# Optimization experiments

Hardware: AMD Instinct MI355X
Metric: run time of the kernel (lower is better)

## Reference

```python
import jax, jax.numpy as jnp
import numpy as np

RATE = 0.5
POLICY = 3
FREQ_MASK = 15
TIME_MASK = 35


def setup_inputs() -> dict:
    key = jax.random.key(0)
    x = jax.random.normal(key, (64, 1, 4000, 128), dtype=jnp.float32)
    return {"x": x}


def _band_mask(key_apply, key_start, b, policy, length, width, rate):
    """Keep-mask [b, length]: True where NOT covered by any random band.

    Matches torch: apply if rand<rate; start = int(rand*(length-width)).
    """
    apply = jax.random.uniform(key_apply, (b, policy)) < rate            # [b,p]
    start = jnp.floor(jax.random.uniform(key_start, (b, policy))
                      * (length - width)).astype(jnp.int32)              # [b,p]
    pos = jnp.arange(length, dtype=jnp.int32)                            # [length]
    hit = (apply[:, :, None]
           & (pos[None, None, :] >= start[:, :, None])
           & (pos[None, None, :] < (start + width)[:, :, None]))        # [b,p,length]
    return ~jnp.any(hit, axis=1)                                         # [b,length]


def reference(x):
    b, c, t, f = x.shape
    kt_a, kt_s, kf_a, kf_s = jax.random.split(jax.random.key(1), 4)
    keep_t = _band_mask(kt_a, kt_s, b, POLICY, t, TIME_MASK, RATE)       # [b,t]
    keep_f = _band_mask(kf_a, kf_s, b, POLICY, f, FREQ_MASK, RATE)       # [b,f]
    mask = (keep_t[:, :, None] & keep_f[:, None, :]).astype(x.dtype)     # [b,t,f]
    return x * mask[:, None, :, :]
```

## Files before the change

### kernel.cpp

```cpp
#include <hip/hip_runtime.h>
#include <stdint.h>


#define RATE 0.5f
#define POLICY 3
#define FREQ_MASK 15
#define TIME_MASK 35
#define B 64
#define T 4000
#define F 128

__device__ __forceinline__ uint32_t rotl32(uint32_t x, int r) {
  return (x << r) | (x >> (32 - r));
}

__device__ __forceinline__ void threefry2x32(uint32_t k0, uint32_t k1,
                                             uint32_t x0, uint32_t x1,
                                             uint32_t* o0, uint32_t* o1) {
  const uint32_t ks2 = k0 ^ k1 ^ 0x1BD11BDAu;
  x0 += k0; x1 += k1;
  x0 += x1; x1 = rotl32(x1, 13); x1 ^= x0;
  x0 += x1; x1 = rotl32(x1, 15); x1 ^= x0;
  x0 += x1; x1 = rotl32(x1, 26); x1 ^= x0;
  x0 += x1; x1 = rotl32(x1,  6); x1 ^= x0;
  x0 += k1; x1 += ks2 + 1u;
  x0 += x1; x1 = rotl32(x1, 17); x1 ^= x0;
  x0 += x1; x1 = rotl32(x1, 29); x1 ^= x0;
  x0 += x1; x1 = rotl32(x1, 16); x1 ^= x0;
  x0 += x1; x1 = rotl32(x1, 24); x1 ^= x0;
  x0 += ks2; x1 += k0 + 2u;
  x0 += x1; x1 = rotl32(x1, 13); x1 ^= x0;
  x0 += x1; x1 = rotl32(x1, 15); x1 ^= x0;
  x0 += x1; x1 = rotl32(x1, 26); x1 ^= x0;
  x0 += x1; x1 = rotl32(x1,  6); x1 ^= x0;
  x0 += k0; x1 += k1 + 3u;
  x0 += x1; x1 = rotl32(x1, 17); x1 ^= x0;
  x0 += x1; x1 = rotl32(x1, 29); x1 ^= x0;
  x0 += x1; x1 = rotl32(x1, 16); x1 ^= x0;
  x0 += x1; x1 = rotl32(x1, 24); x1 ^= x0;
  x0 += k1; x1 += ks2 + 4u;
  x0 += x1; x1 = rotl32(x1, 13); x1 ^= x0;
  x0 += x1; x1 = rotl32(x1, 15); x1 ^= x0;
  x0 += x1; x1 = rotl32(x1, 26); x1 ^= x0;
  x0 += x1; x1 = rotl32(x1,  6); x1 ^= x0;
  x0 += ks2; x1 += k0 + 5u;
  *o0 = x0; *o1 = x1;
}

__device__ __forceinline__ float bits_to_uniform(uint32_t bits) {
  uint32_t fb = (bits >> 9) | 0x3f800000u;
  float f = __uint_as_float(fb) - 1.0f;
  return fmaxf(f, 0.0f);
}

__global__ void band_kernel(int2* __restrict__ tband, int2* __restrict__ fband) {
  const int i = threadIdx.x;
  if (i >= B * POLICY) return;
  const uint32_t K0 = 0u, K1 = 1u;
  uint32_t a0, a1, b0, b1, c0, c1, d0, d1;
  threefry2x32(K0, K1, 0u, 0u, &a0, &a1);
  threefry2x32(K0, K1, 0u, 1u, &b0, &b1);
  threefry2x32(K0, K1, 0u, 2u, &c0, &c1);
  threefry2x32(K0, K1, 0u, 3u, &d0, &d1);

  uint32_t o0, o1;
  threefry2x32(a0, a1, 0u, (uint32_t)i, &o0, &o1);
  const float u_ta = bits_to_uniform(o0 ^ o1);
  threefry2x32(b0, b1, 0u, (uint32_t)i, &o0, &o1);
  const float u_ts = bits_to_uniform(o0 ^ o1);
  threefry2x32(c0, c1, 0u, (uint32_t)i, &o0, &o1);
  const float u_fa = bits_to_uniform(o0 ^ o1);
  threefry2x32(d0, d1, 0u, (uint32_t)i, &o0, &o1);
  const float u_fs = bits_to_uniform(o0 ^ o1);

  const bool ap_t = u_ta < RATE;
  const bool ap_f = u_fa < RATE;
  const int st = (int)floorf(u_ts * (float)(T - TIME_MASK));
  const int sf = (int)floorf(u_fs * (float)(F - FREQ_MASK));
  tband[i] = ap_t ? make_int2(st, st + TIME_MASK) : make_int2(0, 0);
  fband[i] = ap_f ? make_int2(sf, sf + FREQ_MASK) : make_int2(0, 0);
}

__global__ __launch_bounds__(256) void apply_kernel(
    const float4* __restrict__ x, float4* __restrict__ out,
    const int2* __restrict__ tband, const int2* __restrict__ fband) {
  const int b = blockIdx.y;
  const int i = blockIdx.x * 256 + threadIdx.x;
  const int t = i >> 5;
  const int f0 = (i & 31) << 2;

  const int2 tb0 = tband[b * 3 + 0];
  const int2 tb1 = tband[b * 3 + 1];
  const int2 tb2 = tband[b * 3 + 2];
  const bool keep_t = !((t >= tb0.x && t < tb0.y) ||
                        (t >= tb1.x && t < tb1.y) ||
                        (t >= tb2.x && t < tb2.y));
  const int2 fb0 = fband[b * 3 + 0];
  const int2 fb1 = fband[b * 3 + 1];
  const int2 fb2 = fband[b * 3 + 2];

  const long idx = (long)b * (T * F / 4) + i;
  float4 v = x[idx];
  float r[4];
  const float* vp = (const float*)&v;
#pragma unroll
  for (int j = 0; j < 4; ++j) {
    const int f = f0 + j;
    const bool keep_f = !((f >= fb0.x && f < fb0.y) ||
                          (f >= fb1.x && f < fb1.y) ||
                          (f >= fb2.x && f < fb2.y));
    r[j] = (keep_t && keep_f) ? vp[j] : 0.0f;
  }
  out[idx] = *(const float4*)r;
}

extern "C" void kernel_launch(void* const* d_in, const int* in_sizes, int n_in,
                              void* d_out, int out_size, void* d_ws, size_t ws_size,
                              hipStream_t stream) {
  const float4* x = (const float4*)d_in[0];
  float4* out = (float4*)d_out;
  int2* tband = (int2*)d_ws;
  int2* fband = (int2*)((char*)d_ws + B * POLICY * sizeof(int2));

  band_kernel<<<1, 192, 0, stream>>>(tband, fband);

  dim3 grid(T * F / 4 / 256, B);
  apply_kernel<<<grid, 256, 0, stream>>>(x, out, tband, fband);
}
```

Baseline: 219.2 us.

## Fuse RNG band generation into apply kernel with nontemporal multi-row loads

Removes the separate single-block band kernel and recomputes each batch's threefry-derived band parameters inside every block, with 12 threads writing to shared memory. Each thread now handles four float4 elements, all loaded up front with nontemporal loads so the loads overlap the RNG computation, and results are written with nontemporal stores. This removes one kernel launch and its serial dependency, at the cost of redundant RNG work per block and a block-level barrier.

```diff
diff --git a/kernel.cpp b/kernel.cpp
--- a/kernel.cpp
+++ b/kernel.cpp
@@ -9,6 +9,11 @@
 #define B 64
 #define T 4000
 #define F 128
+#define PER_BATCH (T * F / 4)
+#define BLK_CHUNK 1024
+#define ITERS 4
+
+typedef float f32x4 __attribute__((ext_vector_type(4)));
 
 __device__ __forceinline__ uint32_t rotl32(uint32_t x, int r) {
   return (x << r) | (x >> (32 - r));
@@ -53,77 +58,71 @@
   return fmaxf(f, 0.0f);
 }
 
-__global__ void band_kernel(int2* __restrict__ tband, int2* __restrict__ fband) {
-  const int i = threadIdx.x;
-  if (i >= B * POLICY) return;
-  const uint32_t K0 = 0u, K1 = 1u;
-  uint32_t a0, a1, b0, b1, c0, c1, d0, d1;
-  threefry2x32(K0, K1, 0u, 0u, &a0, &a1);
-  threefry2x32(K0, K1, 0u, 1u, &b0, &b1);
-  threefry2x32(K0, K1, 0u, 2u, &c0, &c1);
-  threefry2x32(K0, K1, 0u, 3u, &d0, &d1);
+__global__ __launch_bounds__(256) void specaug_kernel(
+    const f32x4* __restrict__ x, f32x4* __restrict__ out) {
+  __shared__ float us[12];
+  const int b = blockIdx.y;
+  const int tid = threadIdx.x;
 
-  uint32_t o0, o1;
-  threefry2x32(a0, a1, 0u, (uint32_t)i, &o0, &o1);
-  const float u_ta = bits_to_uniform(o0 ^ o1);
-  threefry2x32(b0, b1, 0u, (uint32_t)i, &o0, &o1);
-  const float u_ts = bits_to_uniform(o0 ^ o1);
-  threefry2x32(c0, c1, 0u, (uint32_t)i, &o0, &o1);
-  const float u_fa = bits_to_uniform(o0 ^ o1);
-  threefry2x32(d0, d1, 0u, (uint32_t)i, &o0, &o1);
-  const float u_fs = bits_to_uniform(o0 ^ o1);
+  const size_t base = (size_t)b * PER_BATCH + (size_t)blockIdx.x * BLK_CHUNK + tid;
+  f32x4 v0 = __builtin_nontemporal_load(&x[base + 0 * 256]);
+  f32x4 v1 = __builtin_nontemporal_load(&x[base + 1 * 256]);
+  f32x4 v2 = __builtin_nontemporal_load(&x[base + 2 * 256]);
+  f32x4 v3 = __builtin_nontemporal_load(&x[base + 3 * 256]);
 
-  const bool ap_t = u_ta < RATE;
-  const bool ap_f = u_fa < RATE;
-  const int st = (int)floorf(u_ts * (float)(T - TIME_MASK));
-  const int sf = (int)floorf(u_fs * (float)(F - FREQ_MASK));
-  tband[i] = ap_t ? make_int2(st, st + TIME_MASK) : make_int2(0, 0);
-  fband[i] = ap_f ? make_int2(sf, sf + FREQ_MASK) : make_int2(0, 0);
-}
+  if (tid < 12) {
+    const int d = tid / 3;
+    const int p = tid - d * 3;
+    uint32_t k0, k1, o0, o1;
+    threefry2x32(0u, 1u, 0u, (uint32_t)d, &k0, &k1);
+    threefry2x32(k0, k1, 0u, (uint32_t)(b * 3 + p), &o0, &o1);
+    us[tid] = bits_to_uniform(o0 ^ o1);
+  }
+  __syncthreads();
 
-__global__ __launch_bounds__(256) void apply_kernel(
-    const float4* __restrict__ x, float4* __restrict__ out,
-    const int2* __restrict__ tband, const int2* __restrict__ fband) {
-  const int b = blockIdx.y;
-  const int i = blockIdx.x * 256 + threadIdx.x;
-  const int t = i >> 5;
-  const int f0 = (i & 31) << 2;
+  int tlo[3], flo[3];
+#pragma unroll
+  for (int p = 0; p < 3; ++p) {
+    const bool at = us[0 * 3 + p] < RATE;
+    const bool af = us[2 * 3 + p] < RATE;
+    const int ts = (int)floorf(us[1 * 3 + p] * (float)(T - TIME_MASK));
+    const int fs = (int)floorf(us[3 * 3 + p] * (float)(F - FREQ_MASK));
+    tlo[p] = at ? ts : T;
+    flo[p] = af ? fs : F;
+  }
 
-  const int2 tb0 = tband[b * 3 + 0];
-  const int2 tb1 = tband[b * 3 + 1];
-  const int2 tb2 = tband[b * 3 + 2];
-  const bool keep_t = !((t >= tb0.x && t < tb0.y) ||
-                        (t >= tb1.x && t < tb1.y) ||
-                        (t >= tb2.x && t < tb2.y));
-  const int2 fb0 = fband[b * 3 + 0];
-  const int2 fb1 = fband[b * 3 + 1];
-  const int2 fb2 = fband[b * 3 + 2];
-
-  const long idx = (long)b * (T * F / 4) + i;
-  float4 v = x[idx];
-  float r[4];
-  const float* vp = (const float*)&v;
+  const int f0 = (tid & 31) << 2;
+  bool kf[4];
 #pragma unroll
   for (int j = 0; j < 4; ++j) {
     const int f = f0 + j;
-    const bool keep_f = !((f >= fb0.x && f < fb0.y) ||
-                          (f >= fb1.x && f < fb1.y) ||
-                          (f >= fb2.x && f < fb2.y));
-    r[j] = (keep_t && keep_f) ? vp[j] : 0.0f;
+    kf[j] = !((f >= flo[0] && f < flo[0] + FREQ_MASK) ||
+              (f >= flo[1] && f < flo[1] + FREQ_MASK) ||
+              (f >= flo[2] && f < flo[2] + FREQ_MASK));
   }
-  out[idx] = *(const float4*)r;
+  const int t_base = blockIdx.x * 32 + (tid >> 5);
+
+  f32x4 vv[4] = {v0, v1, v2, v3};
+#pragma unroll
+  for (int i = 0; i < ITERS; ++i) {
+    const int t = t_base + i * 8;
+    const bool kt = !((t >= tlo[0] && t < tlo[0] + TIME_MASK) ||
+                      (t >= tlo[1] && t < tlo[1] + TIME_MASK) ||
+                      (t >= tlo[2] && t < tlo[2] + TIME_MASK));
+    f32x4 r;
+    r.x = (kt && kf[0]) ? vv[i].x : 0.0f;
+    r.y = (kt && kf[1]) ? vv[i].y : 0.0f;
+    r.z = (kt && kf[2]) ? vv[i].z : 0.0f;
+    r.w = (kt && kf[3]) ? vv[i].w : 0.0f;
+    __builtin_nontemporal_store(r, &out[base + i * 256]);
+  }
 }
 
 extern "C" void kernel_launch(void* const* d_in, const int* in_sizes, int n_in,
                               void* d_out, int out_size, void* d_ws, size_t ws_size,
                               hipStream_t stream) {
-  const float4* x = (const float4*)d_in[0];
-  float4* out = (float4*)d_out;
-  int2* tband = (int2*)d_ws;
-  int2* fband = (int2*)((char*)d_ws + B * POLICY * sizeof(int2));
-
-  band_kernel<<<1, 192, 0, stream>>>(tband, fband);
-
-  dim3 grid(T * F / 4 / 256, B);
-  apply_kernel<<<grid, 256, 0, stream>>>(x, out, tband, fband);
+  const f32x4* x = (const f32x4*)d_in[0];
+  f32x4* out = (f32x4*)d_out;
+  dim3 grid(PER_BATCH / BLK_CHUNK, B);
+  specaug_kernel<<<grid, 256, 0, stream>>>(x, out);
 }
```

Measured after the change: 213.9 us. 2.4% less time.
